# Kernel tuning notes

Hardware: AMD Instinct MI355X
Metric: run time of the kernel (lower is better)

## Reference

```python
import jax, jax.numpy as jnp
import numpy as np

B, L, D_IN, D_MODEL, N_LAYERS, D_STATE, D_OUT = 32, 1024, 3, 512, 4, 64, 10


def setup_inputs() -> dict:
    key = jax.random.key(0)
    ks = jax.random.split(key, 6)
    x = jax.random.normal(ks[0], (B, L, D_IN), jnp.float32)
    W_enc = jax.random.normal(ks[1], (D_IN, D_MODEL), jnp.float32) / np.sqrt(D_IN)
    # per-channel log timestep, standard S4 init range [1e-3, 1e-1]
    log_dt = jax.random.uniform(ks[2], (N_LAYERS, D_MODEL), jnp.float32,
                                minval=np.log(1e-3), maxval=np.log(1e-1))
    # S4D-real init: A_n = -(n + 1/2), stored as log of magnitude
    A_log = jnp.broadcast_to(
        jnp.log(0.5 + jnp.arange(D_STATE, dtype=jnp.float32)),
        (N_LAYERS, D_MODEL, D_STATE)) * jnp.ones((), jnp.float32)
    C = jax.random.normal(ks[3], (N_LAYERS, D_MODEL, D_STATE), jnp.float32) / np.sqrt(D_STATE)
    W_ff = jax.random.normal(ks[4], (N_LAYERS, D_MODEL, D_MODEL), jnp.float32) / np.sqrt(D_MODEL)
    W_dec = jax.random.normal(ks[5], (D_MODEL, D_OUT), jnp.float32) / np.sqrt(D_MODEL)
    return dict(x=x, W_enc=W_enc, log_dt=log_dt, A_log=A_log, C=C, W_ff=W_ff, W_dec=W_dec)


def _s4d(x, log_dt, A_log, C):
    """Diagonal real S4D layer (is_real=True, skip=False, identity activation).
    x: (B, L, H); log_dt: (H,); A_log, C: (H, N).
    """
    Lx = x.shape[1]
    dt = jnp.exp(log_dt)                         # (H,)
    A = -jnp.exp(A_log)                          # (H, N) real negative poles
    dtA = dt[:, None] * A                        # (H, N)
    Bbar = (jnp.exp(dtA) - 1.0) / A              # ZOH discretization with B = 1
    # Vandermonde kernel: K[h, l] = sum_n (C*Bbar)[h, n] * exp(dtA[h, n] * l)
    lrange = jnp.arange(Lx, dtype=x.dtype)
    K = jnp.einsum('hn,hnl->hl', C * Bbar, jnp.exp(dtA[:, :, None] * lrange))
    # causal depthwise convolution via FFT (linear conv, pad to 2L)
    n = 2 * Lx
    Kf = jnp.fft.rfft(K, n=n, axis=-1)           # (H, n//2+1)
    xf = jnp.fft.rfft(x, n=n, axis=1)            # (B, n//2+1, H)
    y = jnp.fft.irfft(xf * Kf.T[None], n=n, axis=1)[:, :Lx]
    return y


def reference(x, W_enc, log_dt, A_log, C, W_ff, W_dec):
    h = x @ W_enc                                # (B, L, d_model), bias=False
    for i in range(N_LAYERS):
        h = _s4d(h, log_dt[i], A_log[i], C[i])   # S4D layer
        # dropout is identity at inference; FF block: Linear(no bias) + ReLU
        h = jax.nn.relu(h @ W_ff[i])
    out = h @ W_dec                              # (B, L, d_output)
    return out[:, -1, :]                         # get_last=True -> (B, d_output)
```

## Files before the change

### kernel.cpp

```cpp
#include <hip/hip_runtime.h>
#include <math.h>

#define B_   32
#define L_   1024
#define BT_  (B_*L_)
#define DIN  3
#define H_   512
#define NL   4
#define NS   64
#define DOUT 10
#define CT   128
#define NC   (L_/CT)
#define BH   (B_*H_)

typedef __attribute__((ext_vector_type(8))) _Float16 f16x8;
typedef __attribute__((ext_vector_type(4))) float f32x4;

__device__ inline void gload16(const void* g, void* l) {
    __builtin_amdgcn_global_load_lds((const __attribute__((address_space(1))) void*)g,
                                     (__attribute__((address_space(3))) void*)l, 16, 0, 0);
}

__device__ inline unsigned packh2(float a, float b) {
    unsigned short lo = __builtin_bit_cast(unsigned short, (_Float16)a);
    unsigned short hi = __builtin_bit_cast(unsigned short, (_Float16)b);
    return (unsigned)lo | ((unsigned)hi << 16);
}
__device__ inline float lo16f(unsigned v) {
    return (float)__builtin_bit_cast(_Float16, (unsigned short)(v & 0xffffu));
}
__device__ inline float hi16f(unsigned v) {
    return (float)__builtin_bit_cast(_Float16, (unsigned short)(v >> 16));
}

#define PSW(row, col) ((row) * 64 + ((col) ^ (((row) & 7) << 3)))

#define RAW_BARRIER() do { \
    asm volatile("s_waitcnt lgkmcnt(0)" ::: "memory"); \
    __builtin_amdgcn_s_barrier(); \
    asm volatile("" ::: "memory"); } while (0)

__global__ __launch_bounds__(512, 4) void conv_fused(const float* __restrict__ x,
                                                     const float* __restrict__ Wenc,
                                                     const float* __restrict__ log_dt,
                                                     const float* __restrict__ A_log,
                                                     const float* __restrict__ Cmat,
                                                     const float* __restrict__ WffL,
                                                     _Float16* __restrict__ WTl,
                                                     const _Float16* __restrict__ XT,
                                                     _Float16* __restrict__ YT,
                                                     float* __restrict__ ylast,
                                                     float* __restrict__ outz,
                                                     int layer, int doY) {
    __shared__ __align__(16) _Float16 smem[32768];
    __shared__ float Kl4[4][128];
    __shared__ float Kl[128];
    __shared__ unsigned T32[256];
    __shared__ float dAs[64];
    __shared__ float wps[64];
    __shared__ float rTs[64];
    _Float16* Vl  = smem;
    _Float16* Xh0 = smem + 8192;
    _Float16* Pl  = smem + 16384;
    _Float16* X1r = smem + 24576;
    _Float16* S0l = smem + 24576;
    _Float16* Bp  = smem;

    int bid = blockIdx.x;
    int h = bid >> 1, mh = bid & 1;
    int tid = threadIdx.x;
    int w = tid >> 6, l = tid & 63;
    const int fr = l & 15, q = l >> 4;
    const int wm = w >> 1, wn = w & 1;
    const _Float16* Xh = XT + (size_t)h * BT_ + (size_t)mh * 16384;

    const int c = l & 7, rsub = l >> 3;
    float w0e = 0.f, w1e = 0.f, w2e = 0.f;
    if (layer == 0) { w0e = Wenc[h]; w1e = Wenc[H_ + h]; w2e = Wenc[2 * H_ + h]; }

    if (layer == 0) {
        if (bid == 0 && tid < B_ * DOUT) outz[tid] = 0.f;
#pragma unroll
        for (int s = 0; s < 2; s++) {
            _Float16* dst = s ? X1r : Xh0;
#pragma unroll
            for (int ii = 0; ii < 2; ii++) {
                int t2 = w * 2 + ii;
                int rr = t2 * 8 + rsub;
                int srcc = c ^ (rr & 7);
                int bt = mh * 16384 + rr * 128 + s * 64 + srcc * 8;
                const float* xp = x + (size_t)bt * DIN;
                f16x8 o;
#pragma unroll
                for (int e = 0; e < 8; e++)
                    o[e] = (_Float16)fmaf(xp[e * 3], w0e,
                                     fmaf(xp[e * 3 + 1], w1e, xp[e * 3 + 2] * w2e));
                *(f16x8*)&dst[t2 * 512 + l * 8] = o;
            }
        }
    } else {
#pragma unroll
        for (int s = 0; s < 2; s++) {
            _Float16* dst = s ? X1r : Xh0;
#pragma unroll
            for (int ii = 0; ii < 2; ii++) {
                int t2 = w * 2 + ii;
                int rr = t2 * 8 + rsub;
                int srcc = c ^ (rr & 7);
                gload16(Xh + (size_t)rr * 128 + s * 64 + srcc * 8,
                        &dst[t2 * 512 + l * 8]);
            }
        }
    }

    if (tid < 64) {
        int n = tid;
        float dt  = expf(log_dt[layer * H_ + h]);
        float A   = -expf(A_log[((size_t)layer * H_ + h) * NS + n]);
        float dtA = dt * A;
        float r0  = expf(dtA);
        dAs[n] = dtA;
        wps[n] = Cmat[((size_t)layer * H_ + h) * NS + n] * ((r0 - 1.0f) / A);
        rTs[n] = expf(dtA * (float)CT);
    } else if (layer < 3 && tid < 96) {
        int g = bid * 32 + (tid - 64);
        int n = g >> 6, k8 = g & 63;
        const float* src = WffL + n;
        f16x8 o;
#pragma unroll
        for (int j = 0; j < 8; j++)
            o[j] = (_Float16)src[(size_t)(k8 * 8 + j) * H_];
        *(f16x8*)(WTl + (size_t)n * H_ + k8 * 8) = o;
    }
    RAW_BARRIER();

#pragma unroll
    for (int ii = 0; ii < 2; ii++) {
        int slot = tid + 512 * ii;
        int n = slot >> 4, cc = slot & 15;
        float da = dAs[n];
        int jb = cc * 8;
        float cur  = __expf(da * (float)(127 - jb));
        float rinv = __expf(-da);
        f16x8 vv;
#pragma unroll
        for (int e = 0; e < 8; e++) { vv[e] = (_Float16)cur; cur *= rinv; }
        *(f16x8*)&Vl[n * 128 + ((cc >> 3) * 8 + ((cc & 7) ^ (n & 7))) * 8] = vv;
    }
    if (doY) {
        int t = tid & 127, g = tid >> 7;
        float k = 0.f, d = (float)t;
        for (int n = g * 16; n < g * 16 + 16; n++) k += wps[n] * __expf(dAs[n] * d);
        Kl4[g][t] = k;
    }
    __syncthreads();

    if (doY && tid < 128)
        Kl[tid] = (Kl4[0][tid] + Kl4[1][tid]) + (Kl4[2][tid] + Kl4[3][tid]);

    f16x8 fA[2][2][2];
    f32x4 accP[2][2] = {};
#pragma unroll
    for (int i = 0; i < 2; i++)
#pragma unroll
        for (int kk = 0; kk < 2; kk++) {
            int row = wm * 32 + i * 16 + fr;
            int kc = kk * 4 + q;
            fA[i][0][kk] = *(const f16x8*)&Xh0[row * 64 + ((kc ^ (row & 7)) * 8)];
            fA[i][1][kk] = *(const f16x8*)&X1r[row * 64 + ((kc ^ (row & 7)) * 8)];
        }
#pragma unroll
    for (int s = 0; s < 2; s++)
#pragma unroll
        for (int kk = 0; kk < 2; kk++) {
            int kc = kk * 4 + q;
            f16x8 bv[2];
#pragma unroll
            for (int j = 0; j < 2; j++) {
                int n = wn * 32 + j * 16 + fr;
                bv[j] = *(const f16x8*)&Vl[n * 128 + s * 64 + ((kc ^ (n & 7)) * 8)];
            }
#pragma unroll
            for (int i = 0; i < 2; i++)
#pragma unroll
                for (int j = 0; j < 2; j++)
                    accP[i][j] = __builtin_amdgcn_mfma_f32_16x16x32_f16(
                        fA[i][s][kk], bv[j], accP[i][j], 0, 0, 0);
        }

#pragma unroll
    for (int i = 0; i < 2; i++)
#pragma unroll
        for (int j = 0; j < 2; j++)
#pragma unroll
            for (int tt = 0; tt < 4; tt++) {
                int row = wm * 32 + i * 16 + q * 4 + tt;
                int col = wn * 32 + j * 16 + fr;
                Pl[PSW(row, col)] = (_Float16)accP[i][j][tt];
            }
    __syncthreads();

    if (doY && tid < 256) {
        int d = tid - 128;
        unsigned short lo = 0, hi = 0;
        if (d >= 0) lo = __builtin_bit_cast(unsigned short, (_Float16)Kl[d]);
        if (d >= 1) hi = __builtin_bit_cast(unsigned short, (_Float16)Kl[d - 1]);
        T32[tid] = (unsigned)lo | ((unsigned)hi << 16);
    }

    {
        int bl = tid >> 5, n0 = (tid & 31) * 2;
        float rT0 = rTs[n0], rT1 = rTs[n0 + 1];
        float E0 = 0.f, E1 = 0.f;
        if (doY) {
#pragma unroll
            for (int cc = 0; cc < 8; cc++) {
                int row = bl * 8 + cc;
                *(unsigned*)&S0l[row * 64 + (((n0 >> 3) ^ (row & 7)) * 8) + (n0 & 7)] =
                    packh2(E0, E1);
                unsigned pv = *(const unsigned*)&Pl[PSW(row, n0)];
                E0 = fmaf(rT0, E0, lo16f(pv));
                E1 = fmaf(rT1, E1, hi16f(pv));
            }
        } else {
#pragma unroll
            for (int cc = 0; cc < 8; cc++) {
                int row = bl * 8 + cc;
                unsigned pv = *(const unsigned*)&Pl[PSW(row, n0)];
                E0 = fmaf(rT0, E0, lo16f(pv));
                E1 = fmaf(rT1, E1, hi16f(pv));
            }
            float wE = fmaf(wps[n0], E0, wps[n0 + 1] * E1);
            wE += __shfl_xor(wE, 16);
            wE += __shfl_xor(wE, 8);  wE += __shfl_xor(wE, 4);
            wE += __shfl_xor(wE, 2);  wE += __shfl_xor(wE, 1);
            if ((l & 31) == 0) ylast[(size_t)(mh * 16 + bl) * H_ + h] = wE;
        }
    }
    if (!doY) return;
    __syncthreads();

    {
        int n0 = (tid & 31) * 2, tc = tid >> 5;
        int t0 = tc * 8;
        float ra0 = __expf(dAs[n0]),     ra1 = __expf(dAs[n0 + 1]);
        float c0  = wps[n0] * __expf(dAs[n0] * (float)(t0 + 1));
        float c1  = wps[n0 + 1] * __expf(dAs[n0 + 1] * (float)(t0 + 1));
#pragma unroll
        for (int e = 0; e < 8; e++) {
            *(unsigned*)&Bp[(t0 + e) * 192 + (16 + ((n0 >> 3) ^ e)) * 8 + (n0 & 7)] =
                packh2(c0, c1);
            c0 *= ra0; c1 *= ra1;
        }
    }
#pragma unroll
    for (int ii = 0; ii < 4; ii++) {
        int slot = tid + 512 * ii;
        int t = slot >> 4, cc = slot & 15;
        unsigned* bp32 = (unsigned*)&Bp[t * 192 + ((cc >> 3) * 8 + ((cc & 7) ^ (t & 7))) * 8];
        int base = t - cc * 8 + 128;
#pragma unroll
        for (int p = 0; p < 4; p++)
            bp32[p] = T32[base - 2 * p];
    }
    __syncthreads();

    f32x4 acc[2][4] = {};
#pragma unroll
    for (int s = 0; s < 3; s++)
#pragma unroll
        for (int kk = 0; kk < 2; kk++) {
            int kc = kk * 4 + q;
            f16x8 av[2], bv[4];
#pragma unroll
            for (int i = 0; i < 2; i++) {
                int row = wm * 32 + i * 16 + fr;
                av[i] = (s < 2) ? fA[i][s][kk]
                                : *(const f16x8*)&S0l[row * 64 + ((kc ^ (row & 7)) * 8)];
            }
#pragma unroll
            for (int j = 0; j < 4; j++) {
                int tc = wn * 64 + j * 16 + fr;
                bv[j] = *(const f16x8*)&Bp[tc * 192 + (s * 8 + (kc ^ (tc & 7))) * 8];
            }
#pragma unroll
            for (int i = 0; i < 2; i++)
#pragma unroll
                for (int j = 0; j < 4; j++)
                    acc[i][j] = __builtin_amdgcn_mfma_f32_16x16x32_f16(av[i], bv[j], acc[i][j], 0, 0, 0);
        }

    __syncthreads();
#pragma unroll
    for (int i = 0; i < 2; i++)
#pragma unroll
        for (int j = 0; j < 4; j++)
#pragma unroll
            for (int tt = 0; tt < 4; tt++) {
                int row = wm * 32 + i * 16 + q * 4 + tt;
                int col = wn * 64 + j * 16 + fr;
                smem[row * 136 + col] = (_Float16)acc[i][j][tt];
            }
    __syncthreads();
    _Float16* Yp = YT + (size_t)h * BT_ + (size_t)mh * 16384;
#pragma unroll
    for (int k2 = 0; k2 < 4; k2++) {
        int ch = tid + 512 * k2;
        int r = ch >> 4, c8 = ch & 15;
        *(f16x8*)(Yp + (size_t)r * 128 + c8 * 8) = *(const f16x8*)&smem[r * 136 + c8 * 8];
    }
}

__global__ __launch_bounds__(512, 4) void ffn_gemm_T(
    const _Float16* __restrict__ WT,
    const _Float16* __restrict__ YT,
    _Float16* __restrict__ OT)
{
    __shared__ __align__(16) _Float16 pool[29184];
    _Float16* As0 = pool;
    _Float16* Bs0 = pool + 12288;
    const int tid = threadIdx.x;
    const int l = tid & 63, w = tid >> 6;
    const int bt0 = blockIdx.x * 256;
    const int bn  = blockIdx.y * 128;
    const int srow = l >> 2, schunk = (l & 3) ^ ((l >> 3) & 3);
    const _Float16* ga0 = WT + (size_t)(bn + w * 16 + srow) * H_ + schunk * 8;
    const int btg = tid & 15, kp = (tid >> 4) & 15, bth = tid >> 8;
    const _Float16* gb = YT + (size_t)(kp * 2) * BT_ + bt0 + bth * 128 + btg * 8;

    f16x8 stB[2][2];
    f32x4 acc[4][4] = {};

    auto loadB = [&](int ks, int st) {
        stB[st][0] = *(const f16x8*)(gb + (size_t)(ks * 32) * BT_);
        stB[st][1] = *(const f16x8*)(gb + (size_t)(ks * 32 + 1) * BT_);
    };
    auto stageA = [&](int ks, int buf) {
        gload16(ga0 + ks * 32, As0 + buf * 4096 + w * 512);
    };
    auto writeB = [&](int st, int buf) {
        const int kpc = kp >> 2, kps = kp & 3;
#pragma unroll
        for (int e = 0; e < 8; e++) {
            int row = bth * 128 + btg * 8 + e;
            int off = row * 32 + (row >> 3) * 8 + ((kpc ^ ((row >> 1) & 3)) * 8) + kps * 2;
            _Float16 lo = stB[st][0][e], hi = stB[st][1][e];
            unsigned v = (unsigned)__builtin_bit_cast(unsigned short, lo)
                       | ((unsigned)__builtin_bit_cast(unsigned short, hi) << 16);
            *(unsigned*)&Bs0[buf * 8448 + off] = v;
        }
    };

    loadB(0, 0);
    loadB(1, 1);
    __builtin_amdgcn_sched_barrier(0);
    stageA(0, 0);
    stageA(1, 1);
    writeB(0, 0);
    asm volatile("s_waitcnt vmcnt(1) lgkmcnt(0)" ::: "memory");
    __builtin_amdgcn_s_barrier();
    asm volatile("" ::: "memory");

    const int wm = w >> 2, wn = w & 3;
    const int fr = l & 15, q = l >> 4;
    const int axor = ((fr >> 1) & 3);
#pragma unroll
    for (int ks = 0; ks < 16; ks++) {
        const int a_cur = ks % 3;
        const int b_cur = ks & 1;
        if (ks + 2 < 16) {
            loadB(ks + 2, b_cur);
            __builtin_amdgcn_sched_barrier(0);
            stageA(ks + 2, (ks + 2) % 3);
        }
        f16x8 av[4], bv[4];
#pragma unroll
        for (int i = 0; i < 4; i++) {
            int row = wm * 64 + i * 16 + fr;
            av[i] = *(const f16x8*)&As0[a_cur * 4096 + row * 32 + ((q ^ axor) * 8)];
        }
#pragma unroll
        for (int j = 0; j < 4; j++) {
            int row = wn * 64 + j * 16 + fr;
            bv[j] = *(const f16x8*)&Bs0[b_cur * 8448 + row * 32 + (row >> 3) * 8
                                        + ((q ^ ((row >> 1) & 3)) * 8)];
        }
#pragma unroll
        for (int i = 0; i < 4; i++)
#pragma unroll
            for (int j = 0; j < 4; j++)
                acc[i][j] = __builtin_amdgcn_mfma_f32_16x16x32_f16(av[i], bv[j], acc[i][j], 0, 0, 0);
        if (ks + 1 < 16) {
            writeB((ks + 1) & 1, b_cur ^ 1);
            if (ks + 2 < 16)
                asm volatile("s_waitcnt vmcnt(3) lgkmcnt(0)" ::: "memory");
            else
                asm volatile("s_waitcnt vmcnt(0) lgkmcnt(0)" ::: "memory");
            __builtin_amdgcn_s_barrier();
            asm volatile("" ::: "memory");
        }
    }
    asm volatile("s_waitcnt lgkmcnt(0)" ::: "memory");
    __builtin_amdgcn_s_barrier();
    asm volatile("" ::: "memory");

#pragma unroll
    for (int half = 0; half < 2; half++) {
        if (half) __syncthreads();
        if (wm == half) {
#pragma unroll
            for (int i = 0; i < 4; i++)
#pragma unroll
                for (int j = 0; j < 4; j++)
#pragma unroll
                    for (int tt = 0; tt < 4; tt++) {
                        int r  = i * 16 + q * 4 + tt;
                        int cc = wn * 64 + j * 16 + fr;
                        pool[r * 264 + cc] = (_Float16)fmaxf(acc[i][j][tt], 0.f);
                    }
        }
        __syncthreads();
#pragma unroll
        for (int k2 = 0; k2 < 4; k2++) {
            int ch = tid + 512 * k2;
            int r = ch >> 5, c8 = ch & 31;
            *(f16x8*)(OT + (size_t)(bn + half * 64 + r) * BT_ + bt0 + c8 * 8) =
                *(const f16x8*)&pool[r * 264 + c8 * 8];
        }
    }
}

__global__ __launch_bounds__(512) void final_head2(const float* __restrict__ ylast,
                                                   const float* __restrict__ Wff3,
                                                   const float* __restrict__ Wdec,
                                                   float* __restrict__ out) {
    int bid = blockIdx.x;
    int b = bid >> 3, s = bid & 7;
    int tid = threadIdx.x;
    __shared__ float yrow[H_];
    __shared__ float hpart[8][64];
    yrow[tid] = ylast[(size_t)b * H_ + tid];
    __syncthreads();
    int kg = tid >> 6, tl = tid & 63;
    int t = s * 64 + tl;
    float acc = 0.f;
    const float* wcol = Wff3 + t;
    for (int k = kg * 64; k < kg * 64 + 64; k++)
        acc = fmaf(yrow[k], wcol[(size_t)k * H_], acc);
    hpart[kg][tl] = acc;
    __syncthreads();
    if (tid < 64) {
        float hv = 0.f;
#pragma unroll
        for (int g = 0; g < 8; g++) hv += hpart[g][tid];
        hv = fmaxf(hv, 0.f);
#pragma unroll
        for (int d = 0; d < DOUT; d++) {
            float v = hv * Wdec[(size_t)(s * 64 + tid) * DOUT + d];
            v += __shfl_xor(v, 32); v += __shfl_xor(v, 16);
            v += __shfl_xor(v, 8);  v += __shfl_xor(v, 4);
            v += __shfl_xor(v, 2);  v += __shfl_xor(v, 1);
            if (tid == 0) atomicAdd(&out[(size_t)b * DOUT + d], v);
        }
    }
}

extern "C" void kernel_launch(void* const* d_in, const int* in_sizes, int n_in,
                              void* d_out, int out_size, void* d_ws, size_t ws_size,
                              hipStream_t stream) {
    const float* x      = (const float*)d_in[0];
    const float* Wenc   = (const float*)d_in[1];
    const float* log_dt = (const float*)d_in[2];
    const float* A_log  = (const float*)d_in[3];
    const float* Cmat   = (const float*)d_in[4];
    const float* Wff    = (const float*)d_in[5];
    const float* Wdec   = (const float*)d_in[6];
    float* out = (float*)d_out;

    char* ws = (char*)d_ws;
    _Float16* bufA  = (_Float16*)(ws);
    _Float16* bufB  = (_Float16*)(ws + 33554432);
    _Float16* WT    = (_Float16*)(ws + 68681728);
    float*    ylast = (float*)(ws + 70254592);

    for (int l = 0; l < NL; l++) {
        if (l < NL - 1) {
            conv_fused<<<H_ * 2, 512, 0, stream>>>(x, Wenc, log_dt, A_log, Cmat,
                                                   Wff + (size_t)l * H_ * H_,
                                                   WT + (size_t)l * H_ * H_,
                                                   bufA, bufB, ylast, out, l, 1);
            ffn_gemm_T<<<dim3(BT_ / 256, H_ / 128), 512, 0, stream>>>(
                WT + (size_t)l * H_ * H_, bufB, bufA);
        } else {
            conv_fused<<<H_ * 2, 512, 0, stream>>>(x, Wenc, log_dt, A_log, Cmat,
                                                   Wff + (size_t)l * H_ * H_,
                                                   WT,
                                                   bufA, bufB, ylast, out, l, 0);
            final_head2<<<B_ * 8, 512, 0, stream>>>(ylast, Wff + (size_t)l * H_ * H_, Wdec, out);
        }
    }
}
```

Before: 178.1 us.

## Split conv barrier to overlap second tile load; remap GEMM blocks per XCD

In conv_fused, the full __syncthreads is replaced by a partial vmcnt wait plus barrier. The MFMA work on the first K half (Xh0) now runs before waiting on the remaining global loads for X1r, so those loads overlap with compute. In ffn_gemm_T, the 2D grid becomes a 1D grid of 512 blocks remapped so each XCD (bid&7) gets a contiguous range of token tiles across all four N tiles, improving L2 reuse of the B operand. The hand-written waitcnt counts depend on how many loads are outstanding. If that assumption is wrong, the code could read incomplete data.

```diff
diff --git a/kernel.cpp b/kernel.cpp
--- a/kernel.cpp
+++ b/kernel.cpp
@@ -153,7 +153,9 @@
         for (int n = g * 16; n < g * 16 + 16; n++) k += wps[n] * __expf(dAs[n] * d);
         Kl4[g][t] = k;
     }
-    __syncthreads();
+    asm volatile("s_waitcnt vmcnt(2) lgkmcnt(0)" ::: "memory");
+    __builtin_amdgcn_s_barrier();
+    asm volatile("" ::: "memory");
 
     if (doY && tid < 128)
         Kl[tid] = (Kl4[0][tid] + Kl4[1][tid]) + (Kl4[2][tid] + Kl4[3][tid]);
@@ -167,26 +169,52 @@
             int row = wm * 32 + i * 16 + fr;
             int kc = kk * 4 + q;
             fA[i][0][kk] = *(const f16x8*)&Xh0[row * 64 + ((kc ^ (row & 7)) * 8)];
+        }
+#pragma unroll
+    for (int kk = 0; kk < 2; kk++) {
+        int kc = kk * 4 + q;
+        f16x8 bv[2];
+#pragma unroll
+        for (int j = 0; j < 2; j++) {
+            int n = wn * 32 + j * 16 + fr;
+            bv[j] = *(const f16x8*)&Vl[n * 128 + 0 * 64 + ((kc ^ (n & 7)) * 8)];
+        }
+#pragma unroll
+        for (int i = 0; i < 2; i++)
+#pragma unroll
+            for (int j = 0; j < 2; j++)
+                accP[i][j] = __builtin_amdgcn_mfma_f32_16x16x32_f16(
+                    fA[i][0][kk], bv[j], accP[i][j], 0, 0, 0);
+    }
+
+    asm volatile("s_waitcnt vmcnt(0) lgkmcnt(0)" ::: "memory");
+    __builtin_amdgcn_s_barrier();
+    asm volatile("" ::: "memory");
+
+#pragma unroll
+    for (int i = 0; i < 2; i++)
+#pragma unroll
+        for (int kk = 0; kk < 2; kk++) {
+            int row = wm * 32 + i * 16 + fr;
+            int kc = kk * 4 + q;
             fA[i][1][kk] = *(const f16x8*)&X1r[row * 64 + ((kc ^ (row & 7)) * 8)];
         }
 #pragma unroll
-    for (int s = 0; s < 2; s++)
-#pragma unroll
-        for (int kk = 0; kk < 2; kk++) {
-            int kc = kk * 4 + q;
-            f16x8 bv[2];
-#pragma unroll
-            for (int j = 0; j < 2; j++) {
-                int n = wn * 32 + j * 16 + fr;
-                bv[j] = *(const f16x8*)&Vl[n * 128 + s * 64 + ((kc ^ (n & 7)) * 8)];
-            }
-#pragma unroll
-            for (int i = 0; i < 2; i++)
-#pragma unroll
-                for (int j = 0; j < 2; j++)
-                    accP[i][j] = __builtin_amdgcn_mfma_f32_16x16x32_f16(
-                        fA[i][s][kk], bv[j], accP[i][j], 0, 0, 0);
-        }
+    for (int kk = 0; kk < 2; kk++) {
+        int kc = kk * 4 + q;
+        f16x8 bv[2];
+#pragma unroll
+        for (int j = 0; j < 2; j++) {
+            int n = wn * 32 + j * 16 + fr;
+            bv[j] = *(const f16x8*)&Vl[n * 128 + 1 * 64 + ((kc ^ (n & 7)) * 8)];
+        }
+#pragma unroll
+        for (int i = 0; i < 2; i++)
+#pragma unroll
+            for (int j = 0; j < 2; j++)
+                accP[i][j] = __builtin_amdgcn_mfma_f32_16x16x32_f16(
+                    fA[i][1][kk], bv[j], accP[i][j], 0, 0, 0);
+    }
 
 #pragma unroll
     for (int i = 0; i < 2; i++)
@@ -321,8 +349,10 @@
     _Float16* Bs0 = pool + 12288;
     const int tid = threadIdx.x;
     const int l = tid & 63, w = tid >> 6;
-    const int bt0 = blockIdx.x * 256;
-    const int bn  = blockIdx.y * 128;
+    const int bid = blockIdx.x;
+    const int xcd = bid & 7, slot = bid >> 3;
+    const int bt0 = (xcd * 16 + (slot >> 2)) * 256;
+    const int bn  = (slot & 3) * 128;
     const int srow = l >> 2, schunk = (l & 3) ^ ((l >> 3) & 3);
     const _Float16* ga0 = WT + (size_t)(bn + w * 16 + srow) * H_ + schunk * 8;
     const int btg = tid & 15, kp = (tid >> 4) & 15, bth = tid >> 8;
@@ -489,7 +519,7 @@
                                                    Wff + (size_t)l * H_ * H_,
                                                    WT + (size_t)l * H_ * H_,
                                                    bufA, bufB, ylast, out, l, 1);
-            ffn_gemm_T<<<dim3(BT_ / 256, H_ / 128), 512, 0, stream>>>(
+            ffn_gemm_T<<<512, 512, 0, stream>>>(
                 WT + (size_t)l * H_ * H_, bufB, bufA);
         } else {
             conv_fused<<<H_ * 2, 512, 0, stream>>>(x, Wenc, log_dt, A_log, Cmat,
```

After: 176.1 us, median of 4. No clear change (-1.1%).
